# Performance work log

Measured on AMD Instinct MI355X. Metric: run time of the kernel, lower is better.

The kernel has to match this reference:

```python
import jax, jax.numpy as jnp
import numpy as np

EPS = 1e-5
NH = 8   # num_heads
P = 8    # patch_size (local window)

def layernorm(x, g, b):
    m = jnp.mean(x, axis=-1, keepdims=True)
    v = jnp.var(x, axis=-1, keepdims=True)
    return (x - m) * jax.lax.rsqrt(v + EPS) * g + b

def axis_embed(pos, nf):
    # DETR-style interleaved sin/cos along one axis -> (L, nf)
    dim_t = 10000.0 ** (2.0 * (jnp.arange(nf) // 2).astype(jnp.float32) / nf)
    p = pos[:, None] / dim_t
    return jnp.stack([jnp.sin(p[:, 0::2]), jnp.cos(p[:, 1::2])], axis=-1).reshape(pos.shape[0], nf)

def pos_embed_2d(E, H, W):
    # (H, W, E): first half of channels encode y, second half encode x
    half = E // 2
    ye = axis_embed(jnp.arange(1, H + 1, dtype=jnp.float32), half)
    xe = axis_embed(jnp.arange(1, W + 1, dtype=jnp.float32), half)
    return jnp.concatenate([jnp.broadcast_to(ye[:, None, :], (H, W, half)),
                            jnp.broadcast_to(xe[None, :, :], (H, W, half))], axis=-1)

def pos_embed_1d(L, E):
    # standard sinusoidal, (L, 1, E)
    pos = jnp.arange(L, dtype=jnp.float32)[:, None]
    div = jnp.exp(jnp.arange(0, E, 2, dtype=jnp.float32) * (-np.log(10000.0) / E))
    pe = jnp.zeros((L, E), jnp.float32)
    pe = pe.at[:, 0::2].set(jnp.sin(pos * div)).at[:, 1::2].set(jnp.cos(pos * div))
    return pe[:, None, :]

def mha(q, k, v, Wq, bq, Wk, bk, Wv, bv, Wo, bo, nh):
    # q,k,v: (B, L, C)
    B, Lq, C = q.shape
    hd = C // nh
    qh = (q @ Wq + bq).reshape(B, Lq, nh, hd)
    kh = (k @ Wk + bk).reshape(B, -1, nh, hd)
    vh = (v @ Wv + bv).reshape(B, -1, nh, hd)
    att = jax.nn.softmax(jnp.einsum('bqhd,bkhd->bhqk', qh, kh) / np.sqrt(hd).astype(np.float32), axis=-1)
    out = jnp.einsum('bhqk,bkhd->bqhd', att, vh).reshape(B, Lq, C)
    return out @ Wo + bo

def win_part(x):
    # (N,T,H,W,C) -> (N*T*nWin, P*P, C)
    N, T, H, W, C = x.shape
    x = x.reshape(N, T, H // P, P, W // P, P, C).transpose(0, 1, 2, 4, 3, 5, 6)
    return x.reshape(-1, P * P, C)

def forward(x, g1, b1, g2, b2, g3, b3, g4, b4,
            sWq, sbq, sWk, sbk, sWv, sbv, sWo, sbo,
            cW1, cb1, dwk, dwb, cW2, cb2,
            tWq, tbq, tWk, tbk, tWv, tbv, tWo, tbo,
            fW1, fb1, fW2, fb2):
    N, T, H, W, C = x.shape
    sl_pos = jnp.tile(pos_embed_2d(C, P, P), (H // P, W // P, 1))  # (H,W,C)
    tem_pos = pos_embed_1d(T, C)                                   # (T,1,C)

    # --- spatial local windowed MHSA (q=k=norm1(x+pos), v=norm1(x)) ---
    qk = win_part(layernorm(x + sl_pos, g1, b1))
    vv = win_part(layernorm(x, g1, b1))
    attn = mha(qk, qk, vv, sWq, sbq, sWk, sbk, sWv, sbv, sWo, sbo, NH)
    attn = attn.reshape(N, T, H // P, W // P, P, P, C).transpose(0, 1, 2, 4, 3, 5, 6).reshape(N, T, H, W, C)
    x = x + attn

    # --- Conv FFN: linear -> depthwise 3x3 -> GELU -> linear ---
    h = layernorm(x, g2, b2) @ cW1 + cb1
    Ch = h.shape[-1]
    h = h.reshape(N * T, H, W, Ch).transpose(0, 3, 1, 2)  # NCHW
    h = jax.lax.conv_general_dilated(h, dwk, (1, 1), 'SAME', feature_group_count=Ch,
                                     dimension_numbers=('NCHW', 'OIHW', 'NCHW')) + dwb[None, :, None, None]
    h = jax.nn.gelu(h, approximate=False)
    h = h.transpose(0, 2, 3, 1).reshape(N, T, H, W, Ch)
    x = x + (h @ cW2 + cb2)

    # --- temporal MHSA over T, tokens are (n,h,w) positions ---
    xt = x.transpose(1, 0, 2, 3, 4).reshape(T, N * H * W, C)
    xt = layernorm(xt, g3, b3)
    qt = layernorm(xt + tem_pos, g3, b3).transpose(1, 0, 2)  # (B,T,C)
    vt = layernorm(xt, g3, b3).transpose(1, 0, 2)
    xt = xt + mha(qt, qt, vt, tWq, tbq, tWk, tbk, tWv, tbv, tWo, tbo, NH).transpose(1, 0, 2)

    # --- FFN; original does x = x + drop3(x) (no residual, doubles output) ---
    xt = layernorm(xt, g4, b4)
    xt = jax.nn.gelu(xt @ fW1 + fb1, approximate=False) @ fW2 + fb2
    xt = xt + xt
    return xt.reshape(T, N, H, W, C).transpose(1, 0, 2, 3, 4)

def setup_inputs() -> dict:
    key = jax.random.key(0)
    N, T, H, W, C, DFF, HID = 4, 16, 32, 32, 256, 1024, 1024
    ks = iter(jax.random.split(key, 64))
    def w(*s):
        return jax.random.normal(next(ks), s, jnp.float32) * 0.02
    inp = dict(x=jax.random.normal(next(ks), (N, T, H, W, C), jnp.float32))
    for i in ('1', '2', '3', '4'):
        inp['g' + i] = jnp.ones((C,), jnp.float32)
        inp['b' + i] = jnp.zeros((C,), jnp.float32)
    for pfx in ('s', 't'):
        inp.update({pfx + 'Wq': w(C, C), pfx + 'bq': jnp.zeros((C,), jnp.float32),
                    pfx + 'Wk': w(C, C), pfx + 'bk': jnp.zeros((C,), jnp.float32),
                    pfx + 'Wv': w(C, C), pfx + 'bv': jnp.zeros((C,), jnp.float32),
                    pfx + 'Wo': w(C, C), pfx + 'bo': jnp.zeros((C,), jnp.float32)})
    inp.update(cW1=w(C, HID), cb1=jnp.zeros((HID,), jnp.float32),
               dwk=w(HID, 1, 3, 3), dwb=jnp.zeros((HID,), jnp.float32),
               cW2=w(HID, C), cb2=jnp.zeros((C,), jnp.float32))
    inp.update(fW1=w(C, DFF), fb1=jnp.zeros((DFF,), jnp.float32),
               fW2=w(DFF, C), fb2=jnp.zeros((C,), jnp.float32))
    return inp

def reference(x, g1, b1, g2, b2, g3, b3, g4, b4,
              sWq, sbq, sWk, sbk, sWv, sbv, sWo, sbo,
              cW1, cb1, dwk, dwb, cW2, cb2,
              tWq, tbq, tWk, tbk, tWv, tbv, tWo, tbo,
              fW1, fb1, fW2, fb2):
    return forward(x, g1, b1, g2, b2, g3, b3, g4, b4,
                   sWq, sbq, sWk, sbk, sWv, sbv, sWo, sbo,
                   cW1, cb1, dwk, dwb, cW2, cb2,
                   tWq, tbq, tWk, tbk, tWv, tbv, tWo, tbo,
                   fW1, fb1, fW2, fb2)
```

## Files before the change

kernel.cpp:

```cpp
#include <hip/hip_runtime.h>
#include <hip/hip_bf16.h>

typedef unsigned short u16;
typedef unsigned int u32;
typedef __attribute__((ext_vector_type(4))) float f32x4;
typedef __attribute__((ext_vector_type(8))) short s16x8;

static constexpr int Nn = 4, Tt = 16, Hh = 32, Ww = 32, Cc = 256;
static constexpr int Ltok = Nn * Tt * Hh * Ww;

__device__ __forceinline__ float bf2f(u16 v) {
  union { u32 u; float f; } t; t.u = ((u32)v) << 16; return t.f;
}
__device__ __forceinline__ u16 f2bf(float f) {
  union { u32 u; float f; } t; t.f = f;
  return (u16)((t.u + 0x7fffu + ((t.u >> 16) & 1u)) >> 16);
}
__device__ __forceinline__ ushort4 pack4(float a, float b, float c, float d) {
  ushort4 r; r.x = f2bf(a); r.y = f2bf(b); r.z = f2bf(c); r.w = f2bf(d); return r;
}
__device__ __forceinline__ float geluf(float x) {
  return 0.5f * x * (1.0f + erff(x * 0.70710678118654752f));
}
__device__ __forceinline__ float wsum(float v) {
#pragma unroll
  for (int o = 32; o > 0; o >>= 1) v += __shfl_xor(v, o, 64);
  return v;
}
__device__ __forceinline__ void ln_stats(float a0, float a1, float a2, float a3,
                                         float& m, float& inv) {
  float s  = wsum(a0 + a1 + a2 + a3);
  float s2 = wsum(a0 * a0 + a1 * a1 + a2 * a2 + a3 * a3);
  m = s * (1.0f / 256.0f);
  float v = s2 * (1.0f / 256.0f) - m * m;
  inv = rsqrtf(v + 1e-5f);
}
__device__ __forceinline__ void gload16(const u16* g, u16* l) {
  __builtin_amdgcn_global_load_lds(
      (const __attribute__((address_space(1))) void*)g,
      (__attribute__((address_space(3))) void*)l, 16, 0, 0);
}

__global__ __launch_bounds__(256) void k_pos(float* __restrict__ pe2d,
                                             float* __restrict__ pe1d,
                                             float* __restrict__ dwkT,
                                             float* __restrict__ zb,
                                             const float* __restrict__ dwk) {
  int idx = blockIdx.x * 256 + threadIdx.x;
  if (idx < 16384) {
    int y = idx >> 11, r = idx & 2047, x = r >> 8, c = r & 255;
    float pos; int cc;
    if (c < 128) { pos = (float)(y + 1); cc = c; }
    else         { pos = (float)(x + 1); cc = c - 128; }
    float e = (float)(cc & ~1) * (1.0f / 128.0f);
    float v = pos / powf(10000.0f, e);
    pe2d[idx] = (cc & 1) ? cosf(v) : sinf(v);
  } else if (idx < 20480) {
    int i = idx - 16384;
    int t = i >> 8, c = i & 255;
    float e = (float)(c & ~1) * (1.0f / 256.0f);
    float v = (float)t * powf(10000.0f, -e);
    pe1d[i] = (c & 1) ? cosf(v) : sinf(v);
  } else if (idx < 29696) {
    int i = idx - 20480;
    int c = i & 1023, tap = i >> 10;
    dwkT[tap * 1024 + c] = dwk[c * 9 + tap];
  } else if (idx < 30720) {
    zb[idx - 29696] = 0.0f;
  }
}

__global__ __launch_bounds__(256) void k_wprep(
    const float* __restrict__ s0, const float* __restrict__ s1,
    const float* __restrict__ s2, const float* __restrict__ s3,
    const float* __restrict__ s4, const float* __restrict__ s5,
    const float* __restrict__ s6, const float* __restrict__ s7,
    const float* __restrict__ cW1, const float* __restrict__ cW2,
    const float* __restrict__ fW1, const float* __restrict__ fW2,
    u16* __restrict__ WT) {
  __shared__ float Ls[32][33];
  int b = blockIdx.x;
  const float* src; u16* dst; int Kd, Nd, tb;
  if (b < 512) {
    int seg = b >> 6; tb = b & 63; Kd = 256; Nd = 256;
    const float* tab[8] = {s0, s1, s2, s3, s4, s5, s6, s7};
    src = tab[seg]; dst = WT + seg * 65536;
  } else if (b < 768)  { tb = b - 512;  Kd = 256;  Nd = 1024; src = cW1; dst = WT + 524288; }
  else if (b < 1024)   { tb = b - 768;  Kd = 1024; Nd = 256;  src = cW2; dst = WT + 786432; }
  else if (b < 1280)   { tb = b - 1024; Kd = 256;  Nd = 1024; src = fW1; dst = WT + 1048576; }
  else                 { tb = b - 1280; Kd = 1024; Nd = 256;  src = fW2; dst = WT + 1310720; }
  int nt = Nd >> 5;
  int tk = tb / nt, tn = tb % nt;
  int r = threadIdx.x >> 3, c0 = (threadIdx.x & 7) * 4;
  float4 v = *(const float4*)&src[(size_t)(tk * 32 + r) * Nd + tn * 32 + c0];
  Ls[r][c0] = v.x; Ls[r][c0 + 1] = v.y; Ls[r][c0 + 2] = v.z; Ls[r][c0 + 3] = v.w;
  __syncthreads();
  *(ushort4*)&dst[(size_t)(tn * 32 + r) * Kd + tk * 32 + c0] =
      pack4(Ls[c0][r], Ls[c0 + 1][r], Ls[c0 + 2][r], Ls[c0 + 3][r]);
}

__global__ __launch_bounds__(256) void k_ln1(const float* __restrict__ x,
                                             const float* __restrict__ g,
                                             const float* __restrict__ b,
                                             const float* __restrict__ pe2d,
                                             u16* __restrict__ qk,
                                             u16* __restrict__ vv) {
  int l = blockIdx.x * 4 + (threadIdx.x >> 6);
  int lane = threadIdx.x & 63, c0 = lane * 4;
  int idx = l & 1023, hh = idx >> 5, ww = idx & 31;
  float4 xv = *(const float4*)&x[(size_t)l * Cc + c0];
  float4 pv = *(const float4*)&pe2d[(((hh & 7) << 3) | (ww & 7)) * Cc + c0];
  float q0 = xv.x + pv.x, q1 = xv.y + pv.y, q2 = xv.z + pv.z, q3 = xv.w + pv.w;
  float mx, ix, mq, iq;
  ln_stats(xv.x, xv.y, xv.z, xv.w, mx, ix);
  ln_stats(q0, q1, q2, q3, mq, iq);
  float4 gv = *(const float4*)&g[c0];
  float4 bv = *(const float4*)&b[c0];
  *(ushort4*)&qk[(size_t)l * Cc + c0] =
      pack4((q0 - mq) * iq * gv.x + bv.x, (q1 - mq) * iq * gv.y + bv.y,
            (q2 - mq) * iq * gv.z + bv.z, (q3 - mq) * iq * gv.w + bv.w);
  *(ushort4*)&vv[(size_t)l * Cc + c0] =
      pack4((xv.x - mx) * ix * gv.x + bv.x, (xv.y - mx) * ix * gv.y + bv.y,
            (xv.z - mx) * ix * gv.z + bv.z, (xv.w - mx) * ix * gv.w + bv.w);
}

__global__ __launch_bounds__(256) void k_lnb(const u16* __restrict__ x,
                                             const float* __restrict__ g,
                                             const float* __restrict__ b,
                                             u16* __restrict__ out) {
  int l = blockIdx.x * 4 + (threadIdx.x >> 6);
  int lane = threadIdx.x & 63, c0 = lane * 4;
  ushort4 xv4 = *(const ushort4*)&x[(size_t)l * Cc + c0];
  float x0 = bf2f(xv4.x), x1 = bf2f(xv4.y), x2 = bf2f(xv4.z), x3 = bf2f(xv4.w);
  float m, inv;
  ln_stats(x0, x1, x2, x3, m, inv);
  float4 gv = *(const float4*)&g[c0];
  float4 bv = *(const float4*)&b[c0];
  *(ushort4*)&out[(size_t)l * Cc + c0] =
      pack4((x0 - m) * inv * gv.x + bv.x, (x1 - m) * inv * gv.y + bv.y,
            (x2 - m) * inv * gv.z + bv.z, (x3 - m) * inv * gv.w + bv.w);
}

__global__ __launch_bounds__(256) void k_ln3b(const u16* __restrict__ xa,
                                              const float* __restrict__ g,
                                              const float* __restrict__ b,
                                              const float* __restrict__ pe1d,
                                              u16* __restrict__ xt_base,
                                              u16* __restrict__ qt,
                                              u16* __restrict__ vt) {
  int l = blockIdx.x * 4 + (threadIdx.x >> 6);
  int lane = threadIdx.x & 63, c0 = lane * 4;
  ushort4 xv4 = *(const ushort4*)&xa[(size_t)l * Cc + c0];
  float x0 = bf2f(xv4.x), x1 = bf2f(xv4.y), x2 = bf2f(xv4.z), x3 = bf2f(xv4.w);
  float4 gv = *(const float4*)&g[c0];
  float4 bv = *(const float4*)&b[c0];
  float m, inv;
  ln_stats(x0, x1, x2, x3, m, inv);
  float t0 = (x0 - m) * inv * gv.x + bv.x;
  float t1 = (x1 - m) * inv * gv.y + bv.y;
  float t2 = (x2 - m) * inv * gv.z + bv.z;
  float t3 = (x3 - m) * inv * gv.w + bv.w;
  *(ushort4*)&xt_base[(size_t)l * Cc + c0] = pack4(t0, t1, t2, t3);
  float m2, inv2;
  ln_stats(t0, t1, t2, t3, m2, inv2);
  *(ushort4*)&vt[(size_t)l * Cc + c0] =
      pack4((t0 - m2) * inv2 * gv.x + bv.x, (t1 - m2) * inv2 * gv.y + bv.y,
            (t2 - m2) * inv2 * gv.z + bv.z, (t3 - m2) * inv2 * gv.w + bv.w);
  int tt = (l >> 10) & 15;
  float4 pv = *(const float4*)&pe1d[tt * Cc + c0];
  float s0 = t0 + pv.x, s1 = t1 + pv.y, s2 = t2 + pv.z, s3 = t3 + pv.w;
  float m3, inv3;
  ln_stats(s0, s1, s2, s3, m3, inv3);
  *(ushort4*)&qt[(size_t)l * Cc + c0] =
      pack4((s0 - m3) * inv3 * gv.x + bv.x, (s1 - m3) * inv3 * gv.y + bv.y,
            (s2 - m3) * inv3 * gv.z + bv.z, (s3 - m3) * inv3 * gv.w + bv.w);
}

template <int MODE>
__global__ __launch_bounds__(256) void k_mgemm(const u16* __restrict__ A,
                                               const u16* __restrict__ BT, int ldbt,
                                               const float* __restrict__ bias,
                                               const float* __restrict__ bias2,
                                               const void* __restrict__ res,
                                               void* __restrict__ out,
                                               int M, int N, int K) {
  __shared__ u16 SMEM[2 * 8192];
  const int tid = threadIdx.x;
  const int wave = tid >> 6, lane = tid & 63;
  const int m0 = blockIdx.x * 128, n0 = blockIdx.y * 128;
  const int wm = wave >> 1, wn = wave & 1;
  const int srow = tid >> 2;
  const int scol = (((tid & 3) ^ (srow & 3)) << 3);
  const u16* Ap = A + (size_t)(m0 + srow) * K + scol;
  const u16* Bp = BT + (size_t)(n0 + srow) * ldbt + scol;
  const int ldst = (wave * 64) * 8;
  const int fr = lane & 15, fs = lane >> 4;
  f32x4 acc[4][4] = {};

  auto stage = [&](int buf, int k0) {
    u16* Ad = SMEM + buf * 8192;
    u16* Bd = Ad + 4096;
#pragma unroll
    for (int it = 0; it < 2; ++it) {
      gload16(Ap + (size_t)(it * 64) * K + k0, &Ad[ldst + it * 2048]);
      gload16(Bp + (size_t)(it * 64) * ldbt + k0, &Bd[ldst + it * 2048]);
    }
  };
  auto compute = [&](int buf) {
    const u16* As = SMEM + buf * 8192;
    const u16* Bs = As + 4096;
    s16x8 af[4], bfr[4];
#pragma unroll
    for (int i = 0; i < 4; ++i) {
      int ra = wm * 64 + i * 16 + fr;
      af[i] = *(const s16x8*)&As[ra * 32 + ((fs ^ (ra & 3)) << 3)];
      int rb = wn * 64 + i * 16 + fr;
      bfr[i] = *(const s16x8*)&Bs[rb * 32 + ((fs ^ (rb & 3)) << 3)];
    }
#pragma unroll
    for (int mi = 0; mi < 4; ++mi)
#pragma unroll
      for (int ni = 0; ni < 4; ++ni)
        acc[mi][ni] = __builtin_amdgcn_mfma_f32_16x16x32_bf16(af[mi], bfr[ni],
                                                              acc[mi][ni], 0, 0, 0);
  };

  stage(0, 0);
  __syncthreads();
  const int nt = K >> 5;
  int cur = 0;
  for (int t = 0; t < nt - 1; ++t) {
    stage(cur ^ 1, (t + 1) << 5);
    compute(cur);
    __syncthreads();
    cur ^= 1;
  }
  compute(cur);
  __syncthreads();

  const int orow = fs * 4, ocol = fr;
  if constexpr (MODE == 5) {
    u16* o = (u16*)out;
#pragma unroll
    for (int ni = 0; ni < 4; ++ni) {
      int gc = n0 + wn * 64 + ni * 16 + ocol;
      float bv = bias[gc];
#pragma unroll
      for (int mi = 0; mi < 4; ++mi) {
        int gr = m0 + wm * 64 + mi * 16 + orow;
        *(ushort4*)&o[(size_t)gc * (size_t)M + gr] =
            pack4(acc[mi][ni][0] + bv, acc[mi][ni][1] + bv,
                  acc[mi][ni][2] + bv, acc[mi][ni][3] + bv);
      }
    }
    return;
  }
  float* Wl = (float*)SMEM + wave * 2048;
#pragma unroll
  for (int nh = 0; nh < 2; ++nh) {
#pragma unroll
    for (int mi = 0; mi < 4; ++mi)
#pragma unroll
      for (int nq = 0; nq < 2; ++nq) {
        int ni = nh * 2 + nq;
#pragma unroll
        for (int r = 0; r < 4; ++r) {
          int row = mi * 16 + fs * 4 + r;
          int col = nq * 16 + fr;
          Wl[row * 32 + (col ^ ((row & 7) << 2))] = acc[mi][ni][r];
        }
      }
#pragma unroll
    for (int p = 0; p < 8; ++p) {
      int row = p * 8 + (lane >> 3);
      int c4 = (lane & 7) * 4;
      f32x4 v4 = *(const f32x4*)&Wl[row * 32 + (c4 ^ ((row & 7) << 2))];
      int gr = m0 + wm * 64 + row;
      int gc = n0 + wn * 64 + nh * 32 + c4;
      if constexpr (MODE == 6) {
        bool isq = gc < 256;
        int lc = gc & 255;
        float4 bv4 = *(const float4*)&(isq ? bias : bias2)[lc];
        u16* ob = isq ? (u16*)out : (u16*)res;
        *(ushort4*)&ob[(size_t)gr * 256 + lc] =
            pack4(v4[0] + bv4.x, v4[1] + bv4.y, v4[2] + bv4.z, v4[3] + bv4.w);
      } else {
        float4 bv4 = *(const float4*)&bias[gc];
        float v[4] = {v4[0] + bv4.x, v4[1] + bv4.y, v4[2] + bv4.z, v4[3] + bv4.w};
        const size_t o = (size_t)gr * (size_t)N + gc;
        if constexpr (MODE == 1) {
#pragma unroll
          for (int j = 0; j < 4; ++j) v[j] = geluf(v[j]);
        }
        if constexpr (MODE == 3) {
          ushort4 r4 = *(const ushort4*)&((const u16*)res)[o];
          v[0] += bf2f(r4.x); v[1] += bf2f(r4.y); v[2] += bf2f(r4.z); v[3] += bf2f(r4.w);
        }
        if constexpr (MODE == 7) {
          float4 r4 = *(const float4*)&((const float*)res)[o];
          v[0] += r4.x; v[1] += r4.y; v[2] += r4.z; v[3] += r4.w;
        }
        if constexpr (MODE == 4) {
#pragma unroll
          for (int j = 0; j < 4; ++j) v[j] *= 2.0f;
        }
        if constexpr (MODE == 4) {
          *(float4*)&((float*)out)[o] = make_float4(v[0], v[1], v[2], v[3]);
        } else {
          *(ushort4*)&((u16*)out)[o] = pack4(v[0], v[1], v[2], v[3]);
        }
      }
    }
  }
}

__global__ __launch_bounds__(256) void k_sattn2(const u16* __restrict__ Q,
                                                const u16* __restrict__ Kb,
                                                const u16* __restrict__ VT,
                                                u16* __restrict__ ctx) {
  __shared__ u16 P_lds[4][4096];
  const int tid = threadIdx.x;
  const int wave = tid >> 6, lane = tid & 63;
  const int fr = lane & 15, fs = lane >> 4;
  const int wi = blockIdx.x >> 1;
  const int head = (blockIdx.x & 1) * 4 + wave;
  const int ft = wi >> 4, wy = (wi >> 2) & 3, wx = wi & 3;
  const int base = ft * 1024 + wy * 256 + wx * 8;
  const float scale = 0.17677669529663688f;
  const int ch = head * 32 + fs * 8;
  s16x8 ka[4], qb[4];
#pragma unroll
  for (int t4 = 0; t4 < 4; ++t4) {
    int tok = base + (2 * t4 + (fr >> 3)) * 32 + (fr & 7);
    ka[t4] = *(const s16x8*)&Kb[(size_t)tok * 256 + ch];
    qb[t4] = *(const s16x8*)&Q[(size_t)tok * 256 + ch];
  }
  f32x4 s[4][4] = {};
#pragma unroll
  for (int kt = 0; kt < 4; ++kt)
#pragma unroll
    for (int qt = 0; qt < 4; ++qt)
      s[kt][qt] = __builtin_amdgcn_mfma_f32_16x16x32_bf16(ka[kt], qb[qt], s[kt][qt], 0, 0, 0);
  u16* pw = P_lds[wave];
#pragma unroll
  for (int qt = 0; qt < 4; ++qt) {
    float m = -1e30f;
#pragma unroll
    for (int kt = 0; kt < 4; ++kt)
#pragma unroll
      for (int r = 0; r < 4; ++r) m = fmaxf(m, s[kt][qt][r]);
    m = fmaxf(m, __shfl_xor(m, 16, 64));
    m = fmaxf(m, __shfl_xor(m, 32, 64));
    m *= scale;
    float e[4][4];
    float sum = 0.f;
#pragma unroll
    for (int kt = 0; kt < 4; ++kt)
#pragma unroll
      for (int r = 0; r < 4; ++r) {
        e[kt][r] = __expf(s[kt][qt][r] * scale - m);
        sum += e[kt][r];
      }
    sum += __shfl_xor(sum, 16, 64);
    sum += __shfl_xor(sum, 32, 64);
    float il = 1.0f / sum;
    int q = qt * 16 + fr;
    int rowb = q * 128, sw = (q & 7) << 4;
#pragma unroll
    for (int kt = 0; kt < 4; ++kt)
      *(ushort4*)((char*)pw + ((rowb + kt * 32 + fs * 8) ^ sw)) =
          pack4(e[kt][0] * il, e[kt][1] * il, e[kt][2] * il, e[kt][3] * il);
  }
  f32x4 o[4][2] = {};
#pragma unroll
  for (int ks = 0; ks < 2; ++ks) {
    s16x8 vb[2];
#pragma unroll
    for (int nt = 0; nt < 2; ++nt) {
      int d = head * 32 + nt * 16 + fr;
      int tok = base + (ks * 4 + fs) * 32;
      vb[nt] = *(const s16x8*)&VT[(size_t)d * (size_t)Ltok + tok];
    }
#pragma unroll
    for (int qt = 0; qt < 4; ++qt) {
      int q = qt * 16 + fr;
      s16x8 pa = *(const s16x8*)((char*)pw +
                                 ((q * 128 + ks * 64 + fs * 16) ^ ((q & 7) << 4)));
#pragma unroll
      for (int nt = 0; nt < 2; ++nt)
        o[qt][nt] = __builtin_amdgcn_mfma_f32_16x16x32_bf16(pa, vb[nt], o[qt][nt], 0, 0, 0);
    }
  }
#pragma unroll
  for (int qt = 0; qt < 4; ++qt)
#pragma unroll
    for (int r = 0; r < 4; ++r) {
      int q = qt * 16 + fs * 4 + r;
      int tok = base + (q >> 3) * 32 + (q & 7);
#pragma unroll
      for (int nt = 0; nt < 2; ++nt)
        ctx[(size_t)tok * 256 + head * 32 + nt * 16 + fr] = f2bf(o[qt][nt][r]);
    }
}

__global__ __launch_bounds__(256) void k_tattn2(const u16* __restrict__ Q,
                                                const u16* __restrict__ Kb,
                                                const u16* __restrict__ V,
                                                u16* __restrict__ ctx) {
  __shared__ u16 Vs[16 * 256];
  const int tid = threadIdx.x;
  const int b = blockIdx.x;
  const int n = b >> 10, hw = b & 1023;
  const int tok0 = n * 16384 + hw;
#pragma unroll
  for (int i = 0; i < 2; ++i) {
    int chunk = tid * 2 + i;
    int row = chunk >> 5, c8 = (chunk & 31) * 8;
    *(uint4*)&Vs[row * 256 + c8] =
        *(const uint4*)&V[(size_t)(tok0 + row * 1024) * 256 + c8];
  }
  __syncthreads();
  const int wave = tid >> 6, lane = tid & 63;
  const int fr = lane & 15, fs = lane >> 4;
  const float scale = 0.17677669529663688f;
#pragma unroll
  for (int hg = 0; hg < 2; ++hg) {
    int head = wave + hg * 4;
    int ch = head * 32 + fs * 8;
    size_t go = (size_t)(tok0 + fr * 1024) * 256 + ch;
    s16x8 ka = *(const s16x8*)&Kb[go];
    s16x8 qb = *(const s16x8*)&Q[go];
    f32x4 s = {0.f, 0.f, 0.f, 0.f};
    s = __builtin_amdgcn_mfma_f32_16x16x32_bf16(ka, qb, s, 0, 0, 0);
    float m = fmaxf(fmaxf(s[0], s[1]), fmaxf(s[2], s[3]));
    m = fmaxf(m, __shfl_xor(m, 16, 64));
    m = fmaxf(m, __shfl_xor(m, 32, 64));
    m *= scale;
    float e0 = __expf(s[0] * scale - m), e1 = __expf(s[1] * scale - m);
    float e2 = __expf(s[2] * scale - m), e3 = __expf(s[3] * scale - m);
    float sum = e0 + e1 + e2 + e3;
    sum += __shfl_xor(sum, 16, 64);
    sum += __shfl_xor(sum, 32, 64);
    float il = 1.0f / sum;
    e0 *= il; e1 *= il; e2 *= il; e3 *= il;
    float o[8] = {};
#pragma unroll
    for (int kb = 0; kb < 4; ++kb) {
      int src = kb * 16 + fr;
      float p0 = __shfl(e0, src, 64);
      float p1 = __shfl(e1, src, 64);
      float p2 = __shfl(e2, src, 64);
      float p3 = __shfl(e3, src, 64);
#pragma unroll
      for (int r = 0; r < 4; ++r) {
        float p = r == 0 ? p0 : (r == 1 ? p1 : (r == 2 ? p2 : p3));
        uint4 vv = *(const uint4*)&Vs[(kb * 4 + r) * 256 + ch];
        const u16* vp = (const u16*)&vv;
#pragma unroll
        for (int u = 0; u < 8; ++u) o[u] = fmaf(p, bf2f(vp[u]), o[u]);
      }
    }
    size_t co = (size_t)(tok0 + fr * 1024) * 256 + ch;
    *(ushort4*)&ctx[co] = pack4(o[0], o[1], o[2], o[3]);
    *(ushort4*)&ctx[co + 4] = pack4(o[4], o[5], o[6], o[7]);
  }
}

__global__ __launch_bounds__(256) void k_dwconv(const u16* __restrict__ Hin,
                                                const float* __restrict__ dwkT,
                                                const float* __restrict__ dwb,
                                                int ch0, int oco,
                                                u16* __restrict__ Hout) {
  int flat = blockIdx.x * 256 + threadIdx.x;
  int l = flat >> 5, cg = flat & 31, c0 = cg * 8, tc0 = ch0 + c0;
  int frame = l >> 10, idx = l & 1023, hh = idx >> 5, ww = idx & 31;
  float acc[8];
  *(float4*)&acc[0] = *(const float4*)&dwb[tc0];
  *(float4*)&acc[4] = *(const float4*)&dwb[tc0 + 4];
#pragma unroll
  for (int ky = -1; ky <= 1; ++ky) {
    int h2 = hh + ky;
    if (h2 < 0 || h2 >= 32) continue;
#pragma unroll
    for (int kx = -1; kx <= 1; ++kx) {
      int w2 = ww + kx;
      if (w2 < 0 || w2 >= 32) continue;
      int ln = frame * 1024 + h2 * 32 + w2;
      uint4 hv = *(const uint4*)&Hin[(size_t)ln * 256 + c0];
      const u16* hp = (const u16*)&hv;
      int tap = (ky + 1) * 3 + (kx + 1);
      float wk[8];
      *(float4*)&wk[0] = *(const float4*)&dwkT[tap * 1024 + tc0];
      *(float4*)&wk[4] = *(const float4*)&dwkT[tap * 1024 + tc0 + 4];
#pragma unroll
      for (int u = 0; u < 8; ++u) acc[u] = fmaf(bf2f(hp[u]), wk[u], acc[u]);
    }
  }
  size_t ob = (size_t)l * 512 + oco + c0;
  *(ushort4*)&Hout[ob] = pack4(geluf(acc[0]), geluf(acc[1]), geluf(acc[2]), geluf(acc[3]));
  *(ushort4*)&Hout[ob + 4] = pack4(geluf(acc[4]), geluf(acc[5]), geluf(acc[6]), geluf(acc[7]));
}

extern "C" void kernel_launch(void* const* d_in, const int* in_sizes, int n_in,
                              void* d_out, int out_size, void* d_ws, size_t ws_size,
                              hipStream_t stream) {
  (void)in_sizes; (void)n_in; (void)out_size; (void)ws_size;
  const float* x   = (const float*)d_in[0];
  const float* g1  = (const float*)d_in[1];  const float* b1  = (const float*)d_in[2];
  const float* g2  = (const float*)d_in[3];  const float* b2  = (const float*)d_in[4];
  const float* g3  = (const float*)d_in[5];  const float* b3  = (const float*)d_in[6];
  const float* g4  = (const float*)d_in[7];  const float* b4  = (const float*)d_in[8];
  const float* sWq = (const float*)d_in[9];  const float* sbq = (const float*)d_in[10];
  const float* sWk = (const float*)d_in[11]; const float* sbk = (const float*)d_in[12];
  const float* sWv = (const float*)d_in[13]; const float* sbv = (const float*)d_in[14];
  const float* sWo = (const float*)d_in[15]; const float* sbo = (const float*)d_in[16];
  const float* tWq = (const float*)d_in[17]; const float* tbq = (const float*)d_in[18];
  const float* tWk = (const float*)d_in[19]; const float* tbk = (const float*)d_in[20];
  const float* tWv = (const float*)d_in[21]; const float* tbv = (const float*)d_in[22];
  const float* tWo = (const float*)d_in[23]; const float* tbo = (const float*)d_in[24];
  const float* cW1 = (const float*)d_in[25]; const float* cb1 = (const float*)d_in[26];
  const float* dwk = (const float*)d_in[27]; const float* dwb = (const float*)d_in[28];
  const float* cW2 = (const float*)d_in[29]; const float* cb2 = (const float*)d_in[30];
  const float* fW1 = (const float*)d_in[31]; const float* fb1 = (const float*)d_in[32];
  const float* fW2 = (const float*)d_in[33]; const float* fb2 = (const float*)d_in[34];

  char* ws = (char*)d_ws;
  const size_t MB = 1ull << 20;
  float* PE2D = (float*)(ws);
  float* PE1D = (float*)(ws + (64 << 10));
  float* DWKT = (float*)(ws + (80 << 10));
  float* ZB   = (float*)(ws + (116 << 10));
  u16*   WT   = (u16*)(ws + (128 << 10));
  u16* XA = (u16*)(ws + 4 * MB);
  u16* X1 = (u16*)(ws + 4 * MB);
  u16* B1 = (u16*)(ws + 68 * MB);
  u16* B2 = (u16*)(ws + 100 * MB);
  u16* B3 = (u16*)(ws + 132 * MB);
  u16* B4 = (u16*)(ws + 164 * MB);
  u16* F1 = (u16*)(ws + 4 * MB);
  u16* H1q = B2;
  u16* H2h = B3;

  u16* sWqT = WT;
  u16* sWvT = WT + 2 * 65536;   u16* sWoT = WT + 3 * 65536;
  u16* tWqT = WT + 4 * 65536;
  u16* tWvT = WT + 6 * 65536;   u16* tWoT = WT + 7 * 65536;
  u16* cW1T = WT + 524288;      u16* cW2T = WT + 786432;
  u16* fW1T = WT + 1048576;     u16* fW2T = WT + 1310720;

  dim3 blk(256);
  dim3 gLN(Ltok / 4);
  dim3 g2d(Ltok / 128, 2);
  dim3 g4d(Ltok / 128, 4);
  dim3 g8(Ltok / 128, 8);

  k_pos<<<dim3(120), blk, 0, stream>>>(PE2D, PE1D, DWKT, ZB, dwk);
  k_wprep<<<dim3(1536), blk, 0, stream>>>(sWq, sWk, sWv, sWo, tWq, tWk, tWv, tWo,
                                          cW1, cW2, fW1, fW2, WT);
  k_ln1<<<gLN, blk, 0, stream>>>(x, g1, b1, PE2D, B1, B2);
  k_mgemm<5><<<g2d, blk, 0, stream>>>(B2, sWvT, 256, sbv, nullptr, nullptr, B3,
                                      Ltok, 256, 256);
  k_mgemm<6><<<g4d, blk, 0, stream>>>(B1, sWqT, 256, sbq, sbk, B4, B2,
                                      Ltok, 512, 256);
  k_sattn2<<<dim3(2048), blk, 0, stream>>>(B2, B4, B3, B1);
  k_mgemm<7><<<g2d, blk, 0, stream>>>(B1, sWoT, 256, sbo, nullptr, x, XA,
                                      Ltok, 256, 256);
  k_lnb<<<gLN, blk, 0, stream>>>(XA, g2, b2, B1);
  for (int h = 0; h < 2; ++h) {
    for (int qq = 0; qq < 2; ++qq) {
      int q = h * 2 + qq;
      k_mgemm<0><<<g2d, blk, 0, stream>>>(B1, cW1T + q * 65536, 256, cb1 + q * 256,
                                          nullptr, nullptr, H1q, Ltok, 256, 256);
      k_dwconv<<<dim3(Ltok * 32 / 256), blk, 0, stream>>>(H1q, DWKT, dwb,
                                                          q * 256, qq * 256, H2h);
    }
    k_mgemm<3><<<g2d, blk, 0, stream>>>(H2h, cW2T + h * 512, 1024,
                                        h ? cb2 : ZB, nullptr, XA, XA,
                                        Ltok, 256, 512);
  }
  k_ln3b<<<gLN, blk, 0, stream>>>(XA, g3, b3, PE1D, B1, B2, B3);
  k_mgemm<0><<<g2d, blk, 0, stream>>>(B3, tWvT, 256, tbv, nullptr, nullptr, B4,
                                      Ltok, 256, 256);
  k_mgemm<6><<<g4d, blk, 0, stream>>>(B2, tWqT, 256, tbq, tbk, B3, X1,
                                      Ltok, 512, 256);
  k_tattn2<<<dim3(4096), blk, 0, stream>>>(X1, B3, B4, B2);
  k_mgemm<3><<<g2d, blk, 0, stream>>>(B2, tWoT, 256, tbo, nullptr, B1, B3,
                                      Ltok, 256, 256);
  k_lnb<<<gLN, blk, 0, stream>>>(B3, g4, b4, B4);
  k_mgemm<1><<<g8, blk, 0, stream>>>(B4, fW1T, 256, fb1, nullptr, nullptr, F1,
                                     Ltok, 1024, 256);
  k_mgemm<4><<<g2d, blk, 0, stream>>>(F1, fW2T, 1024, fb2, nullptr, nullptr,
                                      (float*)d_out, Ltok, 256, 1024);
}
```

Baseline: 912.2 us.

## Add weight-stationary GEMM kernel holding 256x256 weights in registers for K=256 projections

Adds a k_sgemm kernel that loads a 256-column weight slice into VGPRs once per block and streams 128 rows of activations through double-buffered LDS in 32-row chunks. All K=256 projections (Q/K/V/O for spatial and temporal attention, conv W1 quarters, FFN W1 quarters) move to it; the fused Q+K launch is split into separate Q and K launches. The aim is to stop re-staging weight tiles through LDS on every k-step and to cut LDS traffic. The cost is heavy register pressure from 32 s16x8 weight fragments per lane, fewer blocks (512), and more kernel launches.

```diff
diff --git a/kernel.cpp b/kernel.cpp
--- a/kernel.cpp
+++ b/kernel.cpp
@@ -177,6 +177,109 @@
 }
 
 template <int MODE>
+__global__ __launch_bounds__(256, 2) void k_sgemm(const u16* __restrict__ A,
+                                                  const u16* __restrict__ WT,
+                                                  const float* __restrict__ bias,
+                                                  const void* __restrict__ res,
+                                                  void* __restrict__ out,
+                                                  int ldout) {
+  __shared__ u16 SMEM[32768];
+  const int tid = threadIdx.x;
+  const int wave = tid >> 6, lane = tid & 63;
+  const int fr = lane & 15, fs = lane >> 4;
+  const int r0base = blockIdx.x * 128;
+  s16x8 wreg[4][8];
+#pragma unroll
+  for (int ni = 0; ni < 4; ++ni)
+#pragma unroll
+    for (int kt = 0; kt < 8; ++kt)
+      wreg[ni][kt] = *(const s16x8*)&WT[(size_t)(wave * 64 + ni * 16 + fr) * 256 +
+                                        kt * 32 + fs * 8];
+  auto stage = [&](int buf, int r0) {
+    u16* Ad = SMEM + buf * 8192;
+#pragma unroll
+    for (int i = 0; i < 4; ++i) {
+      int idx = i * 256 + tid;
+      int row = idx >> 5, s = idx & 31;
+      gload16(A + (size_t)(r0 + row) * 256 + ((s ^ row) << 3), &Ad[idx * 8]);
+    }
+  };
+  float* sc = (float*)(SMEM + 16384) + wave * 2048;
+  stage(0, r0base);
+  __syncthreads();
+#pragma unroll 1
+  for (int c = 0; c < 4; ++c) {
+    if (c < 3) stage((c + 1) & 1, r0base + (c + 1) * 32);
+    const u16* As = SMEM + (c & 1) * 8192;
+    f32x4 acc[2][4] = {};
+#pragma unroll
+    for (int kt = 0; kt < 8; ++kt) {
+      s16x8 a0 = *(const s16x8*)&As[(fr * 32 + ((kt * 4 + fs) ^ fr)) * 8];
+      s16x8 a1 = *(const s16x8*)&As[((16 + fr) * 32 + ((kt * 4 + fs) ^ (16 + fr))) * 8];
+#pragma unroll
+      for (int ni = 0; ni < 4; ++ni) {
+        acc[0][ni] = __builtin_amdgcn_mfma_f32_16x16x32_bf16(a0, wreg[ni][kt],
+                                                             acc[0][ni], 0, 0, 0);
+        acc[1][ni] = __builtin_amdgcn_mfma_f32_16x16x32_bf16(a1, wreg[ni][kt],
+                                                             acc[1][ni], 0, 0, 0);
+      }
+    }
+    const int r0 = r0base + c * 32;
+    if constexpr (MODE == 5) {
+      u16* o = (u16*)out;
+#pragma unroll
+      for (int ni = 0; ni < 4; ++ni) {
+        int gc = wave * 64 + ni * 16 + fr;
+        float bv = bias[gc];
+#pragma unroll
+        for (int mi = 0; mi < 2; ++mi) {
+          int gr = r0 + mi * 16 + fs * 4;
+          *(ushort4*)&o[(size_t)gc * (size_t)Ltok + gr] =
+              pack4(acc[mi][ni][0] + bv, acc[mi][ni][1] + bv,
+                    acc[mi][ni][2] + bv, acc[mi][ni][3] + bv);
+        }
+      }
+    } else {
+#pragma unroll
+      for (int mi = 0; mi < 2; ++mi)
+#pragma unroll
+        for (int ni = 0; ni < 4; ++ni)
+#pragma unroll
+          for (int r = 0; r < 4; ++r) {
+            int row = mi * 16 + fs * 4 + r;
+            int col = ni * 16 + fr;
+            sc[row * 64 + (col ^ ((row & 7) << 3))] = acc[mi][ni][r];
+          }
+#pragma unroll
+      for (int p = 0; p < 8; ++p) {
+        int row = p * 4 + (lane >> 4);
+        int c4 = (lane & 15) * 4;
+        f32x4 v4 = *(const f32x4*)&sc[row * 64 + (c4 ^ ((row & 7) << 3))];
+        int gr = r0 + row;
+        int gc = wave * 64 + c4;
+        float4 bv4 = *(const float4*)&bias[gc];
+        float v[4] = {v4[0] + bv4.x, v4[1] + bv4.y, v4[2] + bv4.z, v4[3] + bv4.w};
+        size_t o = (size_t)gr * (size_t)ldout + gc;
+        if constexpr (MODE == 1) {
+#pragma unroll
+          for (int j = 0; j < 4; ++j) v[j] = geluf(v[j]);
+        }
+        if constexpr (MODE == 3) {
+          ushort4 r4 = *(const ushort4*)&((const u16*)res)[(size_t)gr * 256 + gc];
+          v[0] += bf2f(r4.x); v[1] += bf2f(r4.y); v[2] += bf2f(r4.z); v[3] += bf2f(r4.w);
+        }
+        if constexpr (MODE == 7) {
+          float4 r4 = *(const float4*)&((const float*)res)[(size_t)gr * 256 + gc];
+          v[0] += r4.x; v[1] += r4.y; v[2] += r4.z; v[3] += r4.w;
+        }
+        *(ushort4*)&((u16*)out)[o] = pack4(v[0], v[1], v[2], v[3]);
+      }
+    }
+    __syncthreads();
+  }
+}
+
+template <int MODE>
 __global__ __launch_bounds__(256) void k_mgemm(const u16* __restrict__ A,
                                                const u16* __restrict__ BT, int ldbt,
                                                const float* __restrict__ bias,
@@ -196,7 +299,6 @@
   const int ldst = (wave * 64) * 8;
   const int fr = lane & 15, fs = lane >> 4;
   f32x4 acc[4][4] = {};
-
   auto stage = [&](int buf, int k0) {
     u16* Ad = SMEM + buf * 8192;
     u16* Bd = Ad + 4096;
@@ -224,7 +326,6 @@
         acc[mi][ni] = __builtin_amdgcn_mfma_f32_16x16x32_bf16(af[mi], bfr[ni],
                                                               acc[mi][ni], 0, 0, 0);
   };
-
   stage(0, 0);
   __syncthreads();
   const int nt = K >> 5;
@@ -237,24 +338,6 @@
   }
   compute(cur);
   __syncthreads();
-
-  const int orow = fs * 4, ocol = fr;
-  if constexpr (MODE == 5) {
-    u16* o = (u16*)out;
-#pragma unroll
-    for (int ni = 0; ni < 4; ++ni) {
-      int gc = n0 + wn * 64 + ni * 16 + ocol;
-      float bv = bias[gc];
-#pragma unroll
-      for (int mi = 0; mi < 4; ++mi) {
-        int gr = m0 + wm * 64 + mi * 16 + orow;
-        *(ushort4*)&o[(size_t)gc * (size_t)M + gr] =
-            pack4(acc[mi][ni][0] + bv, acc[mi][ni][1] + bv,
-                  acc[mi][ni][2] + bv, acc[mi][ni][3] + bv);
-      }
-    }
-    return;
-  }
   float* Wl = (float*)SMEM + wave * 2048;
 #pragma unroll
   for (int nh = 0; nh < 2; ++nh) {
@@ -277,38 +360,21 @@
       f32x4 v4 = *(const f32x4*)&Wl[row * 32 + (c4 ^ ((row & 7) << 2))];
       int gr = m0 + wm * 64 + row;
       int gc = n0 + wn * 64 + nh * 32 + c4;
-      if constexpr (MODE == 6) {
-        bool isq = gc < 256;
-        int lc = gc & 255;
-        float4 bv4 = *(const float4*)&(isq ? bias : bias2)[lc];
-        u16* ob = isq ? (u16*)out : (u16*)res;
-        *(ushort4*)&ob[(size_t)gr * 256 + lc] =
-            pack4(v4[0] + bv4.x, v4[1] + bv4.y, v4[2] + bv4.z, v4[3] + bv4.w);
+      float4 bv4 = *(const float4*)&bias[gc];
+      float v[4] = {v4[0] + bv4.x, v4[1] + bv4.y, v4[2] + bv4.z, v4[3] + bv4.w};
+      const size_t o = (size_t)gr * (size_t)N + gc;
+      if constexpr (MODE == 3) {
+        ushort4 r4 = *(const ushort4*)&((const u16*)res)[o];
+        v[0] += bf2f(r4.x); v[1] += bf2f(r4.y); v[2] += bf2f(r4.z); v[3] += bf2f(r4.w);
+      }
+      if constexpr (MODE == 4) {
+#pragma unroll
+        for (int j = 0; j < 4; ++j) v[j] *= 2.0f;
+      }
+      if constexpr (MODE == 4) {
+        *(float4*)&((float*)out)[o] = make_float4(v[0], v[1], v[2], v[3]);
       } else {
-        float4 bv4 = *(const float4*)&bias[gc];
-        float v[4] = {v4[0] + bv4.x, v4[1] + bv4.y, v4[2] + bv4.z, v4[3] + bv4.w};
-        const size_t o = (size_t)gr * (size_t)N + gc;
-        if constexpr (MODE == 1) {
-#pragma unroll
-          for (int j = 0; j < 4; ++j) v[j] = geluf(v[j]);
-        }
-        if constexpr (MODE == 3) {
-          ushort4 r4 = *(const ushort4*)&((const u16*)res)[o];
-          v[0] += bf2f(r4.x); v[1] += bf2f(r4.y); v[2] += bf2f(r4.z); v[3] += bf2f(r4.w);
-        }
-        if constexpr (MODE == 7) {
-          float4 r4 = *(const float4*)&((const float*)res)[o];
-          v[0] += r4.x; v[1] += r4.y; v[2] += r4.z; v[3] += r4.w;
-        }
-        if constexpr (MODE == 4) {
-#pragma unroll
-          for (int j = 0; j < 4; ++j) v[j] *= 2.0f;
-        }
-        if constexpr (MODE == 4) {
-          *(float4*)&((float*)out)[o] = make_float4(v[0], v[1], v[2], v[3]);
-        } else {
-          *(ushort4*)&((u16*)out)[o] = pack4(v[0], v[1], v[2], v[3]);
-        }
+        *(ushort4*)&((u16*)out)[o] = pack4(v[0], v[1], v[2], v[3]);
       }
     }
   }
@@ -541,36 +607,33 @@
   u16* H1q = B2;
   u16* H2h = B3;
 
-  u16* sWqT = WT;
+  u16* sWqT = WT;               u16* sWkT = WT + 65536;
   u16* sWvT = WT + 2 * 65536;   u16* sWoT = WT + 3 * 65536;
-  u16* tWqT = WT + 4 * 65536;
+  u16* tWqT = WT + 4 * 65536;   u16* tWkT = WT + 5 * 65536;
   u16* tWvT = WT + 6 * 65536;   u16* tWoT = WT + 7 * 65536;
   u16* cW1T = WT + 524288;      u16* cW2T = WT + 786432;
   u16* fW1T = WT + 1048576;     u16* fW2T = WT + 1310720;
 
   dim3 blk(256);
   dim3 gLN(Ltok / 4);
+  dim3 gS(512);
   dim3 g2d(Ltok / 128, 2);
-  dim3 g4d(Ltok / 128, 4);
-  dim3 g8(Ltok / 128, 8);
 
   k_pos<<<dim3(120), blk, 0, stream>>>(PE2D, PE1D, DWKT, ZB, dwk);
   k_wprep<<<dim3(1536), blk, 0, stream>>>(sWq, sWk, sWv, sWo, tWq, tWk, tWv, tWo,
                                           cW1, cW2, fW1, fW2, WT);
   k_ln1<<<gLN, blk, 0, stream>>>(x, g1, b1, PE2D, B1, B2);
-  k_mgemm<5><<<g2d, blk, 0, stream>>>(B2, sWvT, 256, sbv, nullptr, nullptr, B3,
-                                      Ltok, 256, 256);
-  k_mgemm<6><<<g4d, blk, 0, stream>>>(B1, sWqT, 256, sbq, sbk, B4, B2,
-                                      Ltok, 512, 256);
+  k_sgemm<5><<<gS, blk, 0, stream>>>(B2, sWvT, sbv, nullptr, B3, 0);
+  k_sgemm<0><<<gS, blk, 0, stream>>>(B1, sWqT, sbq, nullptr, B2, 256);
+  k_sgemm<0><<<gS, blk, 0, stream>>>(B1, sWkT, sbk, nullptr, B4, 256);
   k_sattn2<<<dim3(2048), blk, 0, stream>>>(B2, B4, B3, B1);
-  k_mgemm<7><<<g2d, blk, 0, stream>>>(B1, sWoT, 256, sbo, nullptr, x, XA,
-                                      Ltok, 256, 256);
+  k_sgemm<7><<<gS, blk, 0, stream>>>(B1, sWoT, sbo, x, XA, 256);
   k_lnb<<<gLN, blk, 0, stream>>>(XA, g2, b2, B1);
   for (int h = 0; h < 2; ++h) {
     for (int qq = 0; qq < 2; ++qq) {
       int q = h * 2 + qq;
-      k_mgemm<0><<<g2d, blk, 0, stream>>>(B1, cW1T + q * 65536, 256, cb1 + q * 256,
-                                          nullptr, nullptr, H1q, Ltok, 256, 256);
+      k_sgemm<0><<<gS, blk, 0, stream>>>(B1, cW1T + q * 65536, cb1 + q * 256,
+                                         nullptr, H1q, 256);
       k_dwconv<<<dim3(Ltok * 32 / 256), blk, 0, stream>>>(H1q, DWKT, dwb,
                                                           q * 256, qq * 256, H2h);
     }
@@ -579,16 +642,15 @@
                                         Ltok, 256, 512);
   }
   k_ln3b<<<gLN, blk, 0, stream>>>(XA, g3, b3, PE1D, B1, B2, B3);
-  k_mgemm<0><<<g2d, blk, 0, stream>>>(B3, tWvT, 256, tbv, nullptr, nullptr, B4,
-                                      Ltok, 256, 256);
-  k_mgemm<6><<<g4d, blk, 0, stream>>>(B2, tWqT, 256, tbq, tbk, B3, X1,
-                                      Ltok, 512, 256);
+  k_sgemm<0><<<gS, blk, 0, stream>>>(B3, tWvT, tbv, nullptr, B4, 256);
+  k_sgemm<0><<<gS, blk, 0, stream>>>(B2, tWqT, tbq, nullptr, X1, 256);
+  k_sgemm<0><<<gS, blk, 0, stream>>>(B2, tWkT, tbk, nullptr, B3, 256);
   k_tattn2<<<dim3(4096), blk, 0, stream>>>(X1, B3, B4, B2);
-  k_mgemm<3><<<g2d, blk, 0, stream>>>(B2, tWoT, 256, tbo, nullptr, B1, B3,
-                                      Ltok, 256, 256);
+  k_sgemm<3><<<gS, blk, 0, stream>>>(B2, tWoT, tbo, B1, B3, 256);
   k_lnb<<<gLN, blk, 0, stream>>>(B3, g4, b4, B4);
-  k_mgemm<1><<<g8, blk, 0, stream>>>(B4, fW1T, 256, fb1, nullptr, nullptr, F1,
-                                     Ltok, 1024, 256);
+  for (int q = 0; q < 4; ++q)
+    k_sgemm<1><<<gS, blk, 0, stream>>>(B4, fW1T + q * 65536, fb1 + q * 256,
+                                       nullptr, F1 + q * 256, 1024);
   k_mgemm<4><<<g2d, blk, 0, stream>>>(F1, fW2T, 1024, fb2, nullptr, nullptr,
                                       (float*)d_out, Ltok, 256, 1024);
 }
```

Measured after the change: 785.5 us. -13.9%, faster.
